# Performance work log

Hardware: AMD Instinct MI355X
Metric: run time of the kernel (lower is better)

The kernel has to match this reference:

```python
import jax, jax.numpy as jnp
import numpy as np

C = 192          # filter_channels (= in_channels in this module)
K = 3            # kernel_size
NB = 10          # num_bins of rational-quadratic spline (VITS default)
TB = 5.0         # tail_bound
NF = 4           # number of ConvFlow steps per branch
L = 3            # DDSConv n_layers
LOG2PI = float(np.log(2.0 * np.pi))


def conv1x1(x, w, b):
    # x: (B, Cin, T), w: (Cout, Cin)
    return jnp.einsum('oi,bit->bot', w, x) + b[None, :, None]


def depthwise(x, w, b, dil):
    # x: (B, C, T), w: (C, 1, K), dilated depthwise conv, 'same' padding
    pad = dil * (K - 1) // 2
    y = jax.lax.conv_general_dilated(
        x, w, window_strides=(1,), padding=[(pad, pad)], rhs_dilation=(dil,),
        dimension_numbers=('NCH', 'OIH', 'NCH'), feature_group_count=x.shape[1])
    return y + b[None, :, None]


def layer_norm_c(x, g, b, eps=1e-5):
    # VITS LayerNorm: normalize over the channel axis (axis=1)
    m = jnp.mean(x, axis=1, keepdims=True)
    v = jnp.mean((x - m) ** 2, axis=1, keepdims=True)
    return (x - m) * jax.lax.rsqrt(v + eps) * g[None, :, None] + b[None, :, None]


def dds(x, x_mask, g, dep_w, dep_b, pw_w, pw_b, ln_g, ln_b):
    # DDSConv: dilated depth-separable conv stack with residual
    if g is not None:
        x = x + g
    for i in range(L):
        dil = K ** i
        y = depthwise(x * x_mask, dep_w[i], dep_b[i], dil)
        y = jax.nn.gelu(layer_norm_c(y, ln_g[i, 0], ln_b[i, 0]))
        y = conv1x1(y, pw_w[i], pw_b[i])
        y = jax.nn.gelu(layer_norm_c(y, ln_g[i, 1], ln_b[i, 1]))
        x = x + y  # dropout disabled in deterministic reference
    return x * x_mask


def ew_affine(z, x_mask, m, logs):
    y = (m[None, :, None] + jnp.exp(logs)[None, :, None] * z) * x_mask
    ld = jnp.sum(logs[None, :, None] * x_mask, axis=(1, 2))
    return y, ld


def rqs_forward(x_in, uw, uh, ud):
    # unconstrained rational-quadratic spline, forward direction, linear tails
    mb = 1e-3  # min bin width / height / derivative
    const = float(np.log(np.expm1(1.0 - mb)))
    inside = (x_in >= -TB) & (x_in <= TB)
    ud = jnp.pad(ud, ((0, 0), (0, 0), (0, 0), (1, 1)), constant_values=const)
    wd = jax.nn.softmax(uw, -1); wd = mb + (1.0 - mb * NB) * wd
    cw = jnp.cumsum(wd, -1)
    cw = jnp.concatenate([jnp.zeros_like(cw[..., :1]), cw], -1)
    cw = 2.0 * TB * cw - TB
    cw = cw.at[..., 0].set(-TB).at[..., -1].set(TB)
    wd = cw[..., 1:] - cw[..., :-1]
    ht = jax.nn.softmax(uh, -1); ht = mb + (1.0 - mb * NB) * ht
    ch = jnp.cumsum(ht, -1)
    ch = jnp.concatenate([jnp.zeros_like(ch[..., :1]), ch], -1)
    ch = 2.0 * TB * ch - TB
    ch = ch.at[..., 0].set(-TB).at[..., -1].set(TB)
    ht = ch[..., 1:] - ch[..., :-1]
    dv = mb + jax.nn.softplus(ud)  # (..., NB+1)
    xc = jnp.clip(x_in, -TB, TB)
    idx = jnp.clip(jnp.sum((xc[..., None] >= cw[..., :-1]).astype(jnp.int32), -1) - 1, 0, NB - 1)
    g = lambda a, i: jnp.take_along_axis(a, i[..., None], -1)[..., 0]
    icw, iw, ich, ih = g(cw, idx), g(wd, idx), g(ch, idx), g(ht, idx)
    idelta = ih / iw
    d0, d1 = g(dv, idx), g(dv, idx + 1)
    th = (xc - icw) / iw
    t1m = th * (1.0 - th)
    den = idelta + (d0 + d1 - 2.0 * idelta) * t1m
    out = ich + ih * (idelta * th * th + d0 * t1m) / den
    dnum = idelta * idelta * (d1 * th * th + 2.0 * idelta * t1m + d0 * (1.0 - th) ** 2)
    lad = jnp.log(dnum) - 2.0 * jnp.log(den)
    return jnp.where(inside, out, x_in), jnp.where(inside, lad, 0.0)


def conv_flow(z, x_mask, g, pre_w, pre_b, dep_w, dep_b, pw_w, pw_b, ln_g, ln_b, proj_w, proj_b):
    x0, x1 = z[:, :1], z[:, 1:]  # (B,1,T) each
    h = conv1x1(x0, pre_w, pre_b)
    h = dds(h, x_mask, g, dep_w, dep_b, pw_w, pw_b, ln_g, ln_b)
    h = conv1x1(h, proj_w, proj_b) * x_mask      # (B, 3*NB-1, T)
    B, _, T = h.shape
    h = h.reshape(B, 1, 3 * NB - 1, T).transpose(0, 1, 3, 2)  # (B,1,T,3*NB-1)
    s = 1.0 / np.sqrt(C)
    x1n, lad = rqs_forward(x1, h[..., :NB] * s, h[..., NB:2 * NB] * s, h[..., 2 * NB:])
    zo = jnp.concatenate([x0, x1n], 1) * x_mask
    return zo, jnp.sum(lad * x_mask, axis=(1, 2))


def _forward(x, x_mask, w, e_q, pre_w, pre_b, proj_w, proj_b,
             dds_dep_w, dds_dep_b, dds_pw_w, dds_pw_b, dds_ln_g, dds_ln_b,
             post_pre_w, post_pre_b, post_proj_w, post_proj_b,
             pdds_dep_w, pdds_dep_b, pdds_pw_w, pdds_pw_b, pdds_ln_g, pdds_ln_b,
             aff_m, aff_logs,
             f_pre_w, f_pre_b, f_dep_w, f_dep_b, f_pw_w, f_pw_b, f_ln_g, f_ln_b, f_proj_w, f_proj_b,
             paff_m, paff_logs,
             p_pre_w, p_pre_b, p_dep_w, p_dep_b, p_pw_w, p_pw_b, p_ln_g, p_ln_b, p_proj_w, p_proj_b):
    x = jax.lax.stop_gradient(x)
    h = conv1x1(x, pre_w, pre_b)
    h = dds(h, x_mask, None, dds_dep_w, dds_dep_b, dds_pw_w, dds_pw_b, dds_ln_g, dds_ln_b)
    h = conv1x1(h, proj_w, proj_b) * x_mask
    hw = conv1x1(w, post_pre_w, post_pre_b)
    hw = dds(hw, x_mask, None, pdds_dep_w, pdds_dep_b, pdds_pw_w, pdds_pw_b, pdds_ln_g, pdds_ln_b)
    hw = conv1x1(hw, post_proj_w, post_proj_b) * x_mask
    e = e_q * x_mask
    zq, ldq = ew_affine(e, x_mask, paff_m, paff_logs)
    gp = h + hw
    for i in range(NF):
        zq, ld = conv_flow(zq, x_mask, gp, p_pre_w[i], p_pre_b[i], p_dep_w[i], p_dep_b[i],
                           p_pw_w[i], p_pw_b[i], p_ln_g[i], p_ln_b[i], p_proj_w[i], p_proj_b[i])
        ldq = ldq + ld
        zq = zq[:, ::-1]  # Flip (logdet 0)
    zu, z1 = zq[:, :1], zq[:, 1:]
    u = jax.nn.sigmoid(zu) * x_mask
    z0 = (w - u) * x_mask
    ldq = ldq + jnp.sum((jax.nn.log_sigmoid(zu) + jax.nn.log_sigmoid(-zu)) * x_mask, axis=(1, 2))
    logq = jnp.sum(-0.5 * (LOG2PI + e * e) * x_mask, axis=(1, 2)) - ldq
    y0 = jnp.log(jnp.maximum(z0, 1e-5)) * x_mask  # Log flow
    ldt = jnp.sum(-y0, axis=(1, 2))
    z = jnp.concatenate([y0, z1], 1)
    z, ld = ew_affine(z, x_mask, aff_m, aff_logs)
    ldt = ldt + ld
    for i in range(NF):
        z, ld = conv_flow(z, x_mask, h, f_pre_w[i], f_pre_b[i], f_dep_w[i], f_dep_b[i],
                          f_pw_w[i], f_pw_b[i], f_ln_g[i], f_ln_b[i], f_proj_w[i], f_proj_b[i])
        ldt = ldt + ld
        z = z[:, ::-1]
    nll = jnp.sum(0.5 * (LOG2PI + z * z) * x_mask, axis=(1, 2)) - ldt
    return nll + logq  # (B,)


def setup_inputs() -> dict:
    key = jax.random.key(0)
    ks = jax.random.split(key, 24)
    B, T = 32, 768
    P = 3 * NB - 1
    r = lambda k, shape, s=0.05: jax.random.normal(k, shape, jnp.float32) * s
    d = {}
    d['x'] = jax.random.normal(ks[0], (B, C, T), jnp.float32)
    d['x_mask'] = jnp.ones((B, 1, T), jnp.float32)
    d['w'] = jax.random.uniform(ks[1], (B, 1, T), jnp.float32) * 10.0 + 1.0  # positive durations
    d['e_q'] = jax.random.normal(ks[2], (B, 2, T), jnp.float32)
    d['pre_w'] = r(ks[3], (C, C)); d['pre_b'] = jnp.zeros((C,), jnp.float32)
    d['proj_w'] = r(ks[4], (C, C)); d['proj_b'] = jnp.zeros((C,), jnp.float32)
    d['dds_dep_w'] = r(ks[5], (L, C, 1, K)); d['dds_dep_b'] = jnp.zeros((L, C), jnp.float32)
    d['dds_pw_w'] = r(ks[6], (L, C, C)); d['dds_pw_b'] = jnp.zeros((L, C), jnp.float32)
    d['dds_ln_g'] = jnp.ones((L, 2, C), jnp.float32); d['dds_ln_b'] = jnp.zeros((L, 2, C), jnp.float32)
    d['post_pre_w'] = r(ks[7], (C, 1)); d['post_pre_b'] = jnp.zeros((C,), jnp.float32)
    d['post_proj_w'] = r(ks[8], (C, C)); d['post_proj_b'] = jnp.zeros((C,), jnp.float32)
    d['pdds_dep_w'] = r(ks[9], (L, C, 1, K)); d['pdds_dep_b'] = jnp.zeros((L, C), jnp.float32)
    d['pdds_pw_w'] = r(ks[10], (L, C, C)); d['pdds_pw_b'] = jnp.zeros((L, C), jnp.float32)
    d['pdds_ln_g'] = jnp.ones((L, 2, C), jnp.float32); d['pdds_ln_b'] = jnp.zeros((L, 2, C), jnp.float32)
    d['aff_m'] = r(ks[11], (2,)); d['aff_logs'] = r(ks[12], (2,))
    d['f_pre_w'] = r(ks[13], (NF, C, 1)); d['f_pre_b'] = jnp.zeros((NF, C), jnp.float32)
    d['f_dep_w'] = r(ks[14], (NF, L, C, 1, K)); d['f_dep_b'] = jnp.zeros((NF, L, C), jnp.float32)
    d['f_pw_w'] = r(ks[15], (NF, L, C, C)); d['f_pw_b'] = jnp.zeros((NF, L, C), jnp.float32)
    d['f_ln_g'] = jnp.ones((NF, L, 2, C), jnp.float32); d['f_ln_b'] = jnp.zeros((NF, L, 2, C), jnp.float32)
    d['f_proj_w'] = r(ks[16], (NF, P, C), 0.01); d['f_proj_b'] = jnp.zeros((NF, P), jnp.float32)
    d['paff_m'] = r(ks[17], (2,)); d['paff_logs'] = r(ks[18], (2,))
    d['p_pre_w'] = r(ks[19], (NF, C, 1)); d['p_pre_b'] = jnp.zeros((NF, C), jnp.float32)
    d['p_dep_w'] = r(ks[20], (NF, L, C, 1, K)); d['p_dep_b'] = jnp.zeros((NF, L, C), jnp.float32)
    d['p_pw_w'] = r(ks[21], (NF, L, C, C)); d['p_pw_b'] = jnp.zeros((NF, L, C), jnp.float32)
    d['p_ln_g'] = jnp.ones((NF, L, 2, C), jnp.float32); d['p_ln_b'] = jnp.zeros((NF, L, 2, C), jnp.float32)
    d['p_proj_w'] = r(ks[22], (NF, P, C), 0.01); d['p_proj_b'] = jnp.zeros((NF, P), jnp.float32)
    return d


def reference(x, x_mask, w, e_q, pre_w, pre_b, proj_w, proj_b,
              dds_dep_w, dds_dep_b, dds_pw_w, dds_pw_b, dds_ln_g, dds_ln_b,
              post_pre_w, post_pre_b, post_proj_w, post_proj_b,
              pdds_dep_w, pdds_dep_b, pdds_pw_w, pdds_pw_b, pdds_ln_g, pdds_ln_b,
              aff_m, aff_logs,
              f_pre_w, f_pre_b, f_dep_w, f_dep_b, f_pw_w, f_pw_b, f_ln_g, f_ln_b, f_proj_w, f_proj_b,
              paff_m, paff_logs,
              p_pre_w, p_pre_b, p_dep_w, p_dep_b, p_pw_w, p_pw_b, p_ln_g, p_ln_b, p_proj_w, p_proj_b):
    return _forward(x, x_mask, w, e_q, pre_w, pre_b, proj_w, proj_b,
                    dds_dep_w, dds_dep_b, dds_pw_w, dds_pw_b, dds_ln_g, dds_ln_b,
                    post_pre_w, post_pre_b, post_proj_w, post_proj_b,
                    pdds_dep_w, pdds_dep_b, pdds_pw_w, pdds_pw_b, pdds_ln_g, pdds_ln_b,
                    aff_m, aff_logs,
                    f_pre_w, f_pre_b, f_dep_w, f_dep_b, f_pw_w, f_pw_b, f_ln_g, f_ln_b, f_proj_w, f_proj_b,
                    paff_m, paff_logs,
                    p_pre_w, p_pre_b, p_dep_w, p_dep_b, p_pw_w, p_pw_b, p_ln_g, p_ln_b, p_proj_w, p_proj_b)
```

## Files before the change

### kernel.cpp

```cpp
#include <hip/hip_runtime.h>
#include <math.h>

#define CC 192
#define TTT 768
#define PP 29
#define LOG2PI_F 1.8378770664093453f
#define WSLOT 36864
#define PSW 6144
#define XS 200
#define XS2 196
#define PARL 1728

typedef __attribute__((ext_vector_type(8))) short short8;
typedef __attribute__((ext_vector_type(4))) float floatx4;
typedef __attribute__((ext_vector_type(2))) float float2v;
union Frag { int4 i; short8 s; };

__device__ __forceinline__ float2v fma2(float2v a, float2v b, float2v c){
  return __builtin_elementwise_fma(a, b, c);
}
__device__ __forceinline__ float geluf(float x){
  float u = 1.5957691216057308f * (x + 0.044715f*x*x*x);
  return x * __builtin_amdgcn_rcpf(1.f + __expf(-u));
}
__device__ __forceinline__ float softplus_f(float x){
  return (x > 20.f) ? x : log1pf(__expf(x));
}
__device__ __forceinline__ float logsig_f(float x){
  return -softplus_f(-x);
}
__device__ __forceinline__ unsigned short f2bf(float f){
  unsigned int u = __builtin_bit_cast(unsigned int, f);
  u += 0x7fffu + ((u >> 16) & 1u);
  return (unsigned short)(u >> 16);
}
__device__ __forceinline__ unsigned int packbf2(float a0, float a1){
  return (unsigned int)f2bf(a0) | ((unsigned int)f2bf(a1) << 16);
}
__device__ __forceinline__ void unbf2(unsigned int u, float& lo, float& hi){
  lo = __builtin_bit_cast(float, u << 16);
  hi = __builtin_bit_cast(float, u & 0xffff0000u);
}
__device__ __forceinline__ float2v unbf2v(unsigned int u){
  float2v r;
  r.x = __builtin_bit_cast(float, u << 16);
  r.y = __builtin_bit_cast(float, u & 0xffff0000u);
  return r;
}
__device__ __forceinline__ void unp8(int4 v, float* o){
  unsigned int* p = (unsigned int*)&v;
  unbf2(p[0], o[0], o[1]); unbf2(p[1], o[2], o[3]);
  unbf2(p[2], o[4], o[5]); unbf2(p[3], o[6], o[7]);
}
__device__ __forceinline__ void f4arr(float4 v, float* o){ o[0]=v.x;o[1]=v.y;o[2]=v.z;o[3]=v.w; }
__device__ __forceinline__ float2v pick2(float4 a, float4 b, int p){
  switch(p){
    case 0: return (float2v){a.x, a.y};
    case 1: return (float2v){a.z, a.w};
    case 2: return (float2v){b.x, b.y};
    default: return (float2v){b.z, b.w};
  }
}

__global__ __launch_bounds__(256) void convert_w_k(
    const float* __restrict__ p0, const float* __restrict__ p1,
    const float* __restrict__ p2, const float* __restrict__ p3,
    const float* __restrict__ p4, const float* __restrict__ p5,
    const float* __restrict__ p6, const float* __restrict__ p7,
    const float* __restrict__ p8, unsigned short* __restrict__ Wb){
  int i = blockIdx.x*256 + threadIdx.x;
  const int totalA = 33*WSLOT;
  const int total = totalA + 8*PSW;
  if (i >= total) return;
  if (i < totalA){
    int slot = i / WSLOT, j = i % WSLOT;
    int e = j & 7, lane = (j>>3) & 63, kt = j >> 9;
    int k = kt % 6, tile = kt / 6;
    int co = tile*16 + (lane & 15);
    int kk = k*32 + (lane>>4)*8 + e;
    int r = co*CC + kk;
    const float* src;
    if      (slot == 0) src = p0 + r;
    else if (slot == 1) src = p1 + r;
    else if (slot == 2) src = p2 + r;
    else if (slot < 6)  src = p3 + (size_t)(slot-3)*WSLOT + r;
    else if (slot < 9)  src = p4 + (size_t)(slot-6)*WSLOT + r;
    else if (slot < 21) src = p5 + (size_t)(slot-9)*WSLOT + r;
    else                src = p6 + (size_t)(slot-21)*WSLOT + r;
    Wb[i] = f2bf(*src);
  } else {
    int r2 = i - totalA;
    int ps = r2 / PSW, j = r2 % PSW;
    int e = j & 7, lane = (j>>3) & 63, kt = j >> 9;
    int k = kt % 6, tile = kt / 6;
    int co = tile*16 + (lane & 15); if (co > PP-1) co = PP-1;
    int kk = k*32 + (lane>>4)*8 + e;
    const float* base = (ps < 4) ? (p7 + (size_t)ps*PP*CC) : (p8 + (size_t)(ps-4)*PP*CC);
    Wb[i] = f2bf(base[co*CC + kk]);
  }
}

__global__ __launch_bounds__(256) void pack_par_k(
    const float* __restrict__ dds_dep_w, const float* __restrict__ dds_dep_b,
    const float* __restrict__ dds_ln_g,  const float* __restrict__ dds_ln_b,
    const float* __restrict__ dds_pw_b,
    const float* __restrict__ pdds_dep_w, const float* __restrict__ pdds_dep_b,
    const float* __restrict__ pdds_ln_g,  const float* __restrict__ pdds_ln_b,
    const float* __restrict__ pdds_pw_b,
    const float* __restrict__ p_dep_w, const float* __restrict__ p_dep_b,
    const float* __restrict__ p_ln_g,  const float* __restrict__ p_ln_b,
    const float* __restrict__ p_pw_b,
    const float* __restrict__ f_dep_w, const float* __restrict__ f_dep_b,
    const float* __restrict__ f_ln_g,  const float* __restrict__ f_ln_b,
    const float* __restrict__ f_pw_b,
    float* __restrict__ P){
  int i = blockIdx.x*256 + threadIdx.x;
  const int total = 30*PARL;
  if (i >= total) return;
  int ls = i / PARL, r = i % PARL;
  int arr = r / 192, c = r % 192;
  const float *dep_w, *dep_b, *ln_g, *ln_b, *pw_b;
  int l;
  if (ls < 3){
    l = ls; dep_w = dds_dep_w; dep_b = dds_dep_b; ln_g = dds_ln_g; ln_b = dds_ln_b; pw_b = dds_pw_b;
  } else if (ls < 6){
    l = ls-3; dep_w = pdds_dep_w; dep_b = pdds_dep_b; ln_g = pdds_ln_g; ln_b = pdds_ln_b; pw_b = pdds_pw_b;
  } else if (ls < 18){
    int f = (ls-6)/3; l = (ls-6)%3;
    dep_w = p_dep_w + (size_t)f*3*CC*3; dep_b = p_dep_b + (size_t)f*3*CC;
    ln_g = p_ln_g + (size_t)f*3*2*CC;  ln_b = p_ln_b + (size_t)f*3*2*CC;
    pw_b = p_pw_b + (size_t)f*3*CC;
  } else {
    int f = (ls-18)/3; l = (ls-18)%3;
    dep_w = f_dep_w + (size_t)f*3*CC*3; dep_b = f_dep_b + (size_t)f*3*CC;
    ln_g = f_ln_g + (size_t)f*3*2*CC;  ln_b = f_ln_b + (size_t)f*3*2*CC;
    pw_b = f_pw_b + (size_t)f*3*CC;
  }
  float v;
  if      (arr < 3)  v = dep_w[((size_t)l*CC + c)*3 + arr];
  else if (arr == 3) v = dep_b[(size_t)l*CC + c];
  else if (arr == 4) v = ln_g[((size_t)l*2+0)*CC + c];
  else if (arr == 5) v = ln_b[((size_t)l*2+0)*CC + c];
  else if (arr == 6) v = ln_g[((size_t)l*2+1)*CC + c];
  else if (arr == 7) v = ln_b[((size_t)l*2+1)*CC + c];
  else               v = pw_b[(size_t)l*CC + c];
  P[i] = v;
}

__global__ __launch_bounds__(256) void transpose_x_k(
    const float* __restrict__ x, unsigned short* __restrict__ xT){
  __shared__ unsigned short tile[32*XS];
  int b = blockIdx.y, t0 = blockIdx.x*32, tid = threadIdx.x;
  int tl4 = (tid & 7)*4, cr = tid >> 3;
  #pragma unroll
  for (int rnd=0; rnd<6; rnd++){
    int c = rnd*32 + cr;
    float4 v4 = *(const float4*)(x + ((size_t)b*CC + c)*TTT + t0 + tl4);
    tile[(tl4+0)*XS + c] = f2bf(v4.x);
    tile[(tl4+1)*XS + c] = f2bf(v4.y);
    tile[(tl4+2)*XS + c] = f2bf(v4.z);
    tile[(tl4+3)*XS + c] = f2bf(v4.w);
  }
  __syncthreads();
  #pragma unroll
  for (int k=0;k<3;k++){
    int task = k*256 + tid;
    int row = task/24, cn = task%24;
    *(int4*)(xT + ((size_t)b*TTT + t0 + row)*CC + cn*8) = *(const int4*)&tile[row*XS + cn*8];
  }
}

__global__ __launch_bounds__(256) void conv_cc_k(
    const unsigned short* __restrict__ in, const unsigned short* __restrict__ Wsw,
    const float* __restrict__ bias, const float* __restrict__ mask,
    const unsigned short* __restrict__ addsrc, unsigned short* __restrict__ outb, int mode){
  __shared__ unsigned short bufX[32*XS];
  __shared__ unsigned short bufY[32*XS];
  __shared__ float marr[32];
  int b = blockIdx.y, t0 = blockIdx.x*32, tid = threadIdx.x;
  #pragma unroll
  for (int k=0;k<3;k++){
    int task = k*256 + tid;
    int row = task/24, cn = task%24;
    const unsigned short* src = in + ((size_t)b*TTT + t0 + row)*CC + cn*8;
    *(int4*)&bufX[row*XS + cn*8] = *(const int4*)src;
    if (mode == 2){
      const unsigned short* s2 = addsrc + ((size_t)b*TTT + t0 + row)*CC + cn*8;
      *(int4*)&bufY[row*XS + cn*8] = *(const int4*)s2;
    }
  }
  if (tid >= 128 && tid < 160) marr[tid-128] = mask[(size_t)b*TTT + t0 + (tid-128)];
  __syncthreads();
  int w = tid >> 6, lane = tid & 63;
  int n16 = lane & 15, quad = lane >> 4;
  Frag af[3][6];
  #pragma unroll
  for (int ct=0; ct<3; ct++){
    int tile = w*3 + ct;
    #pragma unroll
    for (int k=0;k<6;k++)
      af[ct][k].i = *(const int4*)(Wsw + ((size_t)(tile*6 + k)*64 + lane)*8);
  }
  floatx4 acc[3][2];
  #pragma unroll
  for (int ct=0;ct<3;ct++)
    #pragma unroll
    for (int tt=0;tt<2;tt++)
      acc[ct][tt] = (floatx4){0.f,0.f,0.f,0.f};
  #pragma unroll
  for (int k=0;k<6;k++){
    Frag bf[2];
    #pragma unroll
    for (int tt=0;tt<2;tt++)
      bf[tt].i = *(const int4*)&bufX[(tt*16+n16)*XS + k*32 + quad*8];
    #pragma unroll
    for (int ct=0;ct<3;ct++)
      #pragma unroll
      for (int tt=0;tt<2;tt++)
        acc[ct][tt] = __builtin_amdgcn_mfma_f32_16x16x32_bf16(af[ct][k].s, bf[tt].s, acc[ct][tt], 0,0,0);
  }
  __syncthreads();
  #pragma unroll
  for (int ct=0;ct<3;ct++){
    int cobase = w*48 + ct*16 + quad*4;
    float4 b4 = *(const float4*)(bias + cobase);
    float ba[4] = {b4.x, b4.y, b4.z, b4.w};
    #pragma unroll
    for (int tt=0;tt<2;tt++){
      int t = tt*16 + n16;
      float mv = (mode >= 1) ? marr[t] : 1.f;
      float av[4] = {0.f,0.f,0.f,0.f};
      if (mode == 2){
        uint2 uy = *(uint2*)&bufY[t*XS + cobase];
        unbf2(uy.x, av[0], av[1]); unbf2(uy.y, av[2], av[3]);
      }
      float hh[4];
      #pragma unroll
      for (int r=0;r<4;r++){
        float v = acc[ct][tt][r] + ba[r];
        if (mode >= 1) v *= mv;
        if (mode == 2) v += av[r];
        hh[r] = v;
      }
      uint2 wv; wv.x = packbf2(hh[0], hh[1]); wv.y = packbf2(hh[2], hh[3]);
      *(uint2*)&bufX[t*XS + cobase] = wv;
    }
  }
  __syncthreads();
  #pragma unroll
  for (int k=0;k<3;k++){
    int task = k*256 + tid;
    int row = task/24, cn = task%24;
    *(int4*)(outb + ((size_t)b*TTT + t0 + row)*CC + cn*8) = *(const int4*)&bufX[row*XS + cn*8];
  }
}

__global__ __launch_bounds__(256,3) void mega_dds_k(
    const unsigned short* __restrict__ in,
    const float* __restrict__ zsrc, int zstride,
    const unsigned short* __restrict__ g,
    unsigned short* __restrict__ outb,
    const float* __restrict__ mask,
    const float* __restrict__ parP,
    const float* __restrict__ pw1, const float* __restrict__ pb1,
    const unsigned short* __restrict__ Wsw,
    int srcmode, int outmode,
    const unsigned short* __restrict__ projW, const float* __restrict__ projB,
    float* __restrict__ z, int zs, float* __restrict__ acco){
  __shared__ unsigned short ping[64*XS2];
  __shared__ float par[2][PARL];
  __shared__ float mrow[64];
  float* pro = par[0];

  int b = blockIdx.y, t0 = blockIdx.x*32, tid = threadIdx.x;
  int ws0 = t0 - 16;
  int w = tid >> 6, lane = tid & 63;
  int n16 = lane & 15, quad = lane >> 4;
  int row = w*16 + n16;
  const float* mkb = mask + (size_t)b*TTT;
  const int dils[3] = {1,3,9};

  if (tid < 64){
    int gt = ws0 + tid;
    bool inr = (gt >= 0) && (gt < TTT);
    int gc = gt < 0 ? 0 : (gt > TTT-1 ? TTT-1 : gt);
    mrow[tid] = inr ? mkb[gc] : 0.f;
  }
  #pragma unroll
  for (int k=0;k<7;k++){
    int i2 = k*256 + tid;
    if (i2 < PARL) par[0][i2] = parP[i2];
  }
  if (srcmode == 0){
    #pragma unroll
    for (int k=0;k<6;k++){
      int task = k*256 + tid;
      int r = task/24, cn = task%24, c0 = cn*8;
      int gt = ws0 + r;
      bool inr = (gt >= 0) && (gt < TTT);
      int gc = gt < 0 ? 0 : (gt > TTT-1 ? TTT-1 : gt);
      float mv = inr ? mkb[gc] : 0.f;
      float hv[8];
      unp8(*(const int4*)(in + ((size_t)b*TTT + gc)*CC + c0), hv);
      uint2 w0, w1;
      w0.x = packbf2(hv[0]*mv, hv[1]*mv); w0.y = packbf2(hv[2]*mv, hv[3]*mv);
      w1.x = packbf2(hv[4]*mv, hv[5]*mv); w1.y = packbf2(hv[6]*mv, hv[7]*mv);
      *(uint2*)&ping[r*XS2 + c0]     = w0;
      *(uint2*)&ping[r*XS2 + c0 + 4] = w1;
    }
  } else {
    #pragma unroll
    for (int k=0;k<6;k++){
      int task = k*256 + tid;
      int r = task/24, cn = task%24, c0 = cn*8;
      int gt = ws0 + r;
      bool inr = (gt >= 0) && (gt < TTT);
      int gc = gt < 0 ? 0 : (gt > TTT-1 ? TTT-1 : gt);
      float mv = inr ? mkb[gc] : 0.f;
      float zv = inr ? zsrc[(size_t)b*zstride + gc] : 0.f;
      float hv[8];
      if (g){
        unp8(*(const int4*)(g + ((size_t)b*TTT + gc)*CC + c0), hv);
      } else {
        #pragma unroll
        for (int e=0;e<8;e++) hv[e] = 0.f;
      }
      float4 pwa = *(const float4*)(pw1 + c0);
      float4 pwb2 = *(const float4*)(pw1 + c0 + 4);
      float4 pba = *(const float4*)(pb1 + c0);
      float4 pbb2 = *(const float4*)(pb1 + c0 + 4);
      float pwv[8], pbv[8];
      f4arr(pwa, pwv); f4arr(pwb2, pwv+4);
      f4arr(pba, pbv); f4arr(pbb2, pbv+4);
      float ov[8];
      #pragma unroll
      for (int e=0;e<8;e++) ov[e] = (hv[e] + fmaf(pwv[e], zv, pbv[e]))*mv;
      uint2 w0, w1;
      w0.x = packbf2(ov[0], ov[1]); w0.y = packbf2(ov[2], ov[3]);
      w1.x = packbf2(ov[4], ov[5]); w1.y = packbf2(ov[6], ov[7]);
      *(uint2*)&ping[r*XS2 + c0]     = w0;
      *(uint2*)&ping[r*XS2 + c0 + 4] = w1;
    }
  }
  __syncthreads();

  #pragma unroll
  for (int l=0; l<3; l++){
    const int dil = dils[l];
    const bool active = (l < 2) || (w == 1) || (w == 2);
    const float* pl = par[l & 1];
    Frag bfr[6];
    floatx4 acc[12];
    if (active){
      int iL = row - dil; iL = iL < 0 ? 0 : iL;
      int iR = row + dil; iR = iR > 63 ? 63 : iR;
      float ml = (row - dil >= 0) ? mrow[iL] : 0.f;
      float mc = mrow[row];
      float mr = (row + dil <= 63) ? mrow[iR] : 0.f;
      float2v ml2 = {ml,ml}, mc2 = {mc,mc}, mr2 = {mr,mr};
      float2v vv[24];
      float s = 0.f, q = 0.f;
      #pragma unroll
      for (int j=0;j<6;j++){
        int kk = j*32 + quad*8;
        uint2 a0 = *(uint2*)&ping[iL*XS2 + kk], a1 = *(uint2*)&ping[iL*XS2 + kk + 4];
        uint2 b0 = *(uint2*)&ping[row*XS2 + kk], b1 = *(uint2*)&ping[row*XS2 + kk + 4];
        uint2 c0v = *(uint2*)&ping[iR*XS2 + kk], c1 = *(uint2*)&ping[iR*XS2 + kk + 4];
        float2v XL[4] = {unbf2v(a0.x), unbf2v(a0.y), unbf2v(a1.x), unbf2v(a1.y)};
        float2v XC[4] = {unbf2v(b0.x), unbf2v(b0.y), unbf2v(b1.x), unbf2v(b1.y)};
        float2v XR[4] = {unbf2v(c0v.x), unbf2v(c0v.y), unbf2v(c1.x), unbf2v(c1.y)};
        float4 w0a = *(const float4*)&pl[kk],       w0b = *(const float4*)&pl[kk+4];
        float4 w1a = *(const float4*)&pl[192+kk],   w1b = *(const float4*)&pl[192+kk+4];
        float4 w2a = *(const float4*)&pl[384+kk],   w2b = *(const float4*)&pl[384+kk+4];
        float4 dba = *(const float4*)&pl[576+kk],   dbb = *(const float4*)&pl[576+kk+4];
        #pragma unroll
        for (int p=0;p<4;p++){
          float2v val = fma2(pick2(w0a,w0b,p), XL[p]*ml2,
                        fma2(pick2(w1a,w1b,p), XC[p]*mc2,
                        fma2(pick2(w2a,w2b,p), XR[p]*mr2, pick2(dba,dbb,p))));
          vv[j*4+p] = val;
          s += val.x + val.y;
          q = fmaf(val.x, val.x, fmaf(val.y, val.y, q));
        }
      }
      s += __shfl_xor(s, 16); s += __shfl_xor(s, 32);
      q += __shfl_xor(q, 16); q += __shfl_xor(q, 32);
      float mm = s*(1.f/CC);
      float rr = rsqrtf(q*(1.f/CC) - mm*mm + 1e-5f);
      {
        float2v mm2 = {mm,mm}, rr2 = {rr,rr};
        #pragma unroll
        for (int j=0;j<6;j++){
          int kk = j*32 + quad*8;
          float4 g0a = *(const float4*)&pl[768+kk], g0b = *(const float4*)&pl[768+kk+4];
          float4 b0a = *(const float4*)&pl[960+kk], b0b = *(const float4*)&pl[960+kk+4];
          unsigned int wwp[4];
          #pragma unroll
          for (int p=0;p<4;p++){
            float2v a = fma2((vv[j*4+p]-mm2)*rr2, pick2(g0a,g0b,p), pick2(b0a,b0b,p));
            wwp[p] = packbf2(geluf(a.x), geluf(a.y));
          }
          bfr[j].i = make_int4((int)wwp[0], (int)wwp[1], (int)wwp[2], (int)wwp[3]);
        }
      }
    }
    __syncthreads();
    if (l < 2){
      const float* src = parP + (size_t)(l+1)*PARL;
      #pragma unroll
      for (int k=0;k<7;k++){
        int i2 = k*256 + tid;
        if (i2 < PARL) par[(l+1)&1][i2] = src[i2];
      }
    }
    if (active){
      const unsigned short* WL = Wsw + (size_t)l*WSLOT;
      #pragma unroll
      for (int tile=0; tile<12; tile++){
        acc[tile] = (floatx4){0.f,0.f,0.f,0.f};
        Frag af[6];
        #pragma unroll
        for (int k=0;k<6;k++)
          af[k].i = *(const int4*)(WL + ((size_t)(tile*6 + k)*64 + lane)*8);
        #pragma unroll
        for (int k=0;k<6;k++)
          acc[tile] = __builtin_amdgcn_mfma_f32_16x16x32_bf16(af[k].s, bfr[k].s, acc[tile], 0,0,0);
      }
      float s2 = 0.f, q2 = 0.f;
      #pragma unroll
      for (int tile=0; tile<12; tile++){
        int co = tile*16 + quad*4;
        float4 pbv = *(const float4*)&pl[1536+co];
        float pba[4]; f4arr(pbv, pba);
        #pragma unroll
        for (int r=0;r<4;r++){
          acc[tile][r] += pba[r];
          float x = acc[tile][r];
          s2 += x; q2 = fmaf(x, x, q2);
        }
      }
      s2 += __shfl_xor(s2, 16); s2 += __shfl_xor(s2, 32);
      q2 += __shfl_xor(q2, 16); q2 += __shfl_xor(q2, 32);
      float cmP = s2*(1.f/CC);
      float crP = rsqrtf(q2*(1.f/CC) - cmP*cmP + 1e-5f);
      float2v cm2 = {cmP,cmP}, cr2 = {crP,crP};
      #pragma unroll
      for (int tile=0; tile<12; tile++){
        int co = tile*16 + quad*4;
        float4 g1v = *(const float4*)&pl[1152+co];
        float4 b1v = *(const float4*)&pl[1344+co];
        uint2 ux = *(uint2*)&ping[row*XS2 + co];
        float2v x01 = unbf2v(ux.x), x23 = unbf2v(ux.y);
        float2v v01 = {acc[tile][0], acc[tile][1]};
        float2v v23 = {acc[tile][2], acc[tile][3]};
        float2v a01 = fma2((v01-cm2)*cr2, (float2v){g1v.x,g1v.y}, (float2v){b1v.x,b1v.y});
        float2v a23 = fma2((v23-cm2)*cr2, (float2v){g1v.z,g1v.w}, (float2v){b1v.z,b1v.w});
        uint2 wv;
        wv.x = packbf2(x01.x + geluf(a01.x), x01.y + geluf(a01.y));
        wv.y = packbf2(x23.x + geluf(a23.x), x23.y + geluf(a23.y));
        *(uint2*)&ping[row*XS2 + co] = wv;
      }
    }
    __syncthreads();
  }

  if (outmode == 0){
    #pragma unroll
    for (int k=0;k<3;k++){
      int task = k*256 + tid;
      int r = task/24, cn = task%24, c0 = cn*8;
      uint2 u0 = *(uint2*)&ping[(16+r)*XS2 + c0];
      uint2 u1 = *(uint2*)&ping[(16+r)*XS2 + c0 + 4];
      *(int4*)(outb + ((size_t)b*TTT + t0 + r)*CC + c0) =
          make_int4((int)u0.x, (int)u0.y, (int)u1.x, (int)u1.y);
    }
    return;
  }

  if (w == 1 || w == 2){
    Frag bfp[6];
    #pragma unroll
    for (int k=0;k<6;k++){
      int kk = k*32 + quad*8;
      uint2 u0 = *(uint2*)&ping[row*XS2 + kk];
      uint2 u1 = *(uint2*)&ping[row*XS2 + kk + 4];
      bfp[k].i = make_int4((int)u0.x, (int)u0.y, (int)u1.x, (int)u1.y);
    }
    floatx4 acc2[2];
    acc2[0] = (floatx4){0.f,0.f,0.f,0.f};
    acc2[1] = (floatx4){0.f,0.f,0.f,0.f};
    #pragma unroll
    for (int ct2=0; ct2<2; ct2++){
      #pragma unroll
      for (int k=0;k<6;k++){
        Frag af;
        af.i = *(const int4*)(projW + ((size_t)(ct2*6 + k)*64 + lane)*8);
        acc2[ct2] = __builtin_amdgcn_mfma_f32_16x16x32_bf16(af.s, bfp[k].s, acc2[ct2], 0,0,0);
      }
    }
    int rt = row - 16;
    float mv = mrow[row];
    #pragma unroll
    for (int ct2=0; ct2<2; ct2++){
      int cobase = ct2*16 + quad*4;
      #pragma unroll
      for (int r=0;r<4;r++){
        int co = cobase + r;
        if (co < PP) pro[rt*30 + co] = (acc2[ct2][r] + projB[co]) * mv;
      }
    }
  }
  __syncthreads();
  if (tid < 32){
    const float scv = 0.07216878364870323f;
    int tg = t0 + tid;
    float m = mrow[16+tid];
    float* z0p = z + ((size_t)b*2 + zs)*TTT + tg;
    float* z1p = z + ((size_t)b*2 + (1-zs))*TTT + tg;
    float xs = *z1p;
    float uw[10], uh[10], ud[9];
    #pragma unroll
    for (int k=0;k<10;k++) uw[k]=pro[tid*30+k]*scv;
    #pragma unroll
    for (int k=0;k<10;k++) uh[k]=pro[tid*30+10+k]*scv;
    #pragma unroll
    for (int k=0;k<9;k++)  ud[k]=pro[tid*30+20+k];
    bool inside = (xs >= -5.f) && (xs <= 5.f);
    float xc = fminf(fmaxf(xs,-5.f),5.f);
    float mx=uw[0];
    #pragma unroll
    for (int k=1;k<10;k++) mx=fmaxf(mx,uw[k]);
    float sw=0.f; float wd[10];
    #pragma unroll
    for (int k=0;k<10;k++){ wd[k]=__expf(uw[k]-mx); sw+=wd[k]; }
    float invw = 1.f/sw;
    #pragma unroll
    for (int k=0;k<10;k++) wd[k]=fmaf(0.99f*invw, wd[k], 1e-3f);
    float mh=uh[0];
    #pragma unroll
    for (int k=1;k<10;k++) mh=fmaxf(mh,uh[k]);
    float sh=0.f; float ht[10];
    #pragma unroll
    for (int k=0;k<10;k++){ ht[k]=__expf(uh[k]-mh); sh+=ht[k]; }
    float invh = 1.f/sh;
    #pragma unroll
    for (int k=0;k<10;k++) ht[k]=fmaf(0.99f*invh, ht[k], 1e-3f);
    float cw=-5.f, icw=-5.f, iw=1.f; int idx=0;
    #pragma unroll
    for (int i2=0;i2<10;i2++){
      float nw = (i2==9) ? 5.f : fmaf(10.f, wd[i2], cw);
      if (cw <= xc){ idx=i2; icw=cw; iw=nw-cw; }
      cw=nw;
    }
    float ch=-5.f, ich=-5.f, ih=1.f;
    #pragma unroll
    for (int i2=0;i2<10;i2++){
      float nh = (i2==9) ? 5.f : fmaf(10.f, ht[i2], ch);
      if (i2==idx){ ich=ch; ih=nh-ch; }
      ch=nh;
    }
    const float UDC = logf(expm1f(0.999f));
    float d0=1.f, d1=1.f;
    #pragma unroll
    for (int k=0;k<11;k++){
      float uu = (k==0 || k==10) ? UDC : ud[k-1];
      float dk = 1e-3f + softplus_f(uu);
      if (k==idx)   d0=dk;
      if (k==idx+1) d1=dk;
    }
    float idel = ih/iw;
    float th = (xc-icw)/iw;
    float t1m = th*(1.f-th);
    float den = idel + (d0+d1-2.f*idel)*t1m;
    float outv = ich + ih*(idel*th*th + d0*t1m)/den;
    float omt = 1.f-th;
    float dnum = idel*idel*(d1*th*th + 2.f*idel*t1m + d0*omt*omt);
    float lad = logf(dnum) - 2.f*logf(den);
    float y = inside ? outv : xs;
    lad = inside ? lad : 0.f;
    *z1p = y*m;
    *z0p = (*z0p)*m;
    float lm = lad*m;
    lm += __shfl_xor(lm, 1); lm += __shfl_xor(lm, 2);
    lm += __shfl_xor(lm, 4); lm += __shfl_xor(lm, 8);
    lm += __shfl_xor(lm, 16);
    if (tid == 0) atomicAdd(acco + b, -lm);
  }
}

__global__ __launch_bounds__(256) void init_z_k(
    const float* __restrict__ e_q, const float* __restrict__ mask,
    const float* __restrict__ pm, const float* __restrict__ pl,
    float* __restrict__ z, float* __restrict__ acc){
  __shared__ float red[256];
  int b = blockIdx.y; int t = blockIdx.x*256 + threadIdx.x;
  float m = mask[(size_t)b*TTT + t];
  float pl0=pl[0], pl1=pl[1];
  float e0 = e_q[((size_t)b*2+0)*TTT + t]*m;
  float e1 = e_q[((size_t)b*2+1)*TTT + t]*m;
  z[((size_t)b*2+0)*TTT + t] = fmaf(__expf(pl0), e0, pm[0])*m;
  z[((size_t)b*2+1)*TTT + t] = fmaf(__expf(pl1), e1, pm[1])*m;
  float contrib = -0.5f*(LOG2PI_F + e0*e0)*m - 0.5f*(LOG2PI_F + e1*e1)*m - (pl0+pl1)*m;
  int tid = threadIdx.x;
  red[tid] = contrib;
  __syncthreads();
  for (int o=128;o>0;o>>=1){ if (tid<o) red[tid]+=red[tid+o]; __syncthreads(); }
  if (tid==0) atomicAdd(acc+b, red[0]);
}

__global__ __launch_bounds__(256) void final_pre_k(
    float* __restrict__ z, const float* __restrict__ w_in, const float* __restrict__ mask,
    const float* __restrict__ am, const float* __restrict__ al, float* __restrict__ acc){
  __shared__ float red[256];
  int b = blockIdx.y; int t = blockIdx.x*256 + threadIdx.x;
  float m = mask[(size_t)b*TTT + t];
  float zu  = z[((size_t)b*2+0)*TTT + t];
  float z1v = z[((size_t)b*2+1)*TTT + t];
  float wv  = w_in[(size_t)b*TTT + t];
  float u  = m / (1.f + __expf(-zu));
  float z0 = (wv - u)*m;
  float y0 = logf(fmaxf(z0, 1e-5f))*m;
  float al0=al[0], al1=al[1];
  z[((size_t)b*2+0)*TTT + t] = fmaf(__expf(al0), y0,  am[0])*m;
  z[((size_t)b*2+1)*TTT + t] = fmaf(__expf(al1), z1v, am[1])*m;
  float contrib = -(logsig_f(zu)+logsig_f(-zu))*m + y0 - (al0+al1)*m;
  int tid = threadIdx.x;
  red[tid] = contrib;
  __syncthreads();
  for (int o=128;o>0;o>>=1){ if (tid<o) red[tid]+=red[tid+o]; __syncthreads(); }
  if (tid==0) atomicAdd(acc+b, red[0]);
}

__global__ __launch_bounds__(256) void final_post_k(
    const float* __restrict__ z, const float* __restrict__ mask, float* __restrict__ acc){
  __shared__ float red[256];
  int b = blockIdx.y; int t = blockIdx.x*256 + threadIdx.x;
  float m = mask[(size_t)b*TTT + t];
  float z0 = z[((size_t)b*2+0)*TTT + t];
  float z1 = z[((size_t)b*2+1)*TTT + t];
  float contrib = 0.5f*(LOG2PI_F + z0*z0)*m + 0.5f*(LOG2PI_F + z1*z1)*m;
  int tid = threadIdx.x;
  red[tid] = contrib;
  __syncthreads();
  for (int o=128;o>0;o>>=1){ if (tid<o) red[tid]+=red[tid+o]; __syncthreads(); }
  if (tid==0) atomicAdd(acc+b, red[0]);
}

__global__ void write_out_k(const float* __restrict__ acc, float* __restrict__ out, int n){
  int i = threadIdx.x;
  if (i < n) out[i] = acc[i];
}

extern "C" void kernel_launch(void* const* d_in, const int* in_sizes, int n_in,
                              void* d_out, int out_size, void* d_ws, size_t ws_size,
                              hipStream_t stream){
  (void)n_in; (void)out_size; (void)ws_size;
  const float* x         = (const float*)d_in[0];
  const float* mask      = (const float*)d_in[1];
  const float* w_in      = (const float*)d_in[2];
  const float* e_q       = (const float*)d_in[3];
  const float* pre_w     = (const float*)d_in[4];
  const float* pre_b     = (const float*)d_in[5];
  const float* proj_w    = (const float*)d_in[6];
  const float* proj_b    = (const float*)d_in[7];
  const float* dds_dep_w = (const float*)d_in[8];
  const float* dds_dep_b = (const float*)d_in[9];
  const float* dds_pw_w  = (const float*)d_in[10];
  const float* dds_pw_b  = (const float*)d_in[11];
  const float* dds_ln_g  = (const float*)d_in[12];
  const float* dds_ln_b  = (const float*)d_in[13];
  const float* post_pre_w  = (const float*)d_in[14];
  const float* post_pre_b  = (const float*)d_in[15];
  const float* post_proj_w = (const float*)d_in[16];
  const float* post_proj_b = (const float*)d_in[17];
  const float* pdds_dep_w  = (const float*)d_in[18];
  const float* pdds_dep_b  = (const float*)d_in[19];
  const float* pdds_pw_w   = (const float*)d_in[20];
  const float* pdds_pw_b   = (const float*)d_in[21];
  const float* pdds_ln_g   = (const float*)d_in[22];
  const float* pdds_ln_b   = (const float*)d_in[23];
  const float* aff_m    = (const float*)d_in[24];
  const float* aff_logs = (const float*)d_in[25];
  const float* f_pre_w  = (const float*)d_in[26];
  const float* f_pre_b  = (const float*)d_in[27];
  const float* f_dep_w  = (const float*)d_in[28];
  const float* f_dep_b  = (const float*)d_in[29];
  const float* f_pw_w   = (const float*)d_in[30];
  const float* f_pw_b   = (const float*)d_in[31];
  const float* f_ln_g   = (const float*)d_in[32];
  const float* f_ln_b   = (const float*)d_in[33];
  const float* f_proj_w = (const float*)d_in[34];
  const float* f_proj_b = (const float*)d_in[35];
  const float* paff_m    = (const float*)d_in[36];
  const float* paff_logs = (const float*)d_in[37];
  const float* p_pre_w  = (const float*)d_in[38];
  const float* p_pre_b  = (const float*)d_in[39];
  const float* p_dep_w  = (const float*)d_in[40];
  const float* p_dep_b  = (const float*)d_in[41];
  const float* p_pw_w   = (const float*)d_in[42];
  const float* p_pw_b   = (const float*)d_in[43];
  const float* p_ln_g   = (const float*)d_in[44];
  const float* p_ln_b   = (const float*)d_in[45];
  const float* p_proj_w = (const float*)d_in[46];
  const float* p_proj_b = (const float*)d_in[47];

  int Bn = in_sizes[0] / (CC*TTT);
  size_t big2 = (size_t)Bn*CC*TTT;
  unsigned short* xT = (unsigned short*)d_ws;
  unsigned short* A  = xT + big2;
  unsigned short* Bb = A  + big2;
  unsigned short* H  = Bb + big2;
  unsigned short* GP = H  + big2;
  unsigned short* Wb = GP + big2;
  size_t wtot = 33*(size_t)WSLOT + 8*(size_t)PSW;
  float* parP = (float*)(Wb + ((wtot + 7) & ~(size_t)7));
  float* zbuf = parP + 30*(size_t)PARL;
  float* acc  = zbuf + (size_t)Bn*2*TTT;

  hipMemsetAsync(acc, 0, Bn*sizeof(float), stream);
  convert_w_k<<<(int)((wtot + 255)/256), 256, 0, stream>>>(
      pre_w, proj_w, post_proj_w, dds_pw_w, pdds_pw_w, p_pw_w, f_pw_w,
      p_proj_w, f_proj_w, Wb);
  pack_par_k<<<(30*PARL + 255)/256, 256, 0, stream>>>(
      dds_dep_w, dds_dep_b, dds_ln_g, dds_ln_b, dds_pw_b,
      pdds_dep_w, pdds_dep_b, pdds_ln_g, pdds_ln_b, pdds_pw_b,
      p_dep_w, p_dep_b, p_ln_g, p_ln_b, p_pw_b,
      f_dep_w, f_dep_b, f_ln_g, f_ln_b, f_pw_b, parP);

  dim3 g32(TTT/32, Bn), g256(TTT/256, Bn);
  dim3 b256(256);

  unsigned short* W_pre      = Wb + 0*(size_t)WSLOT;
  unsigned short* W_proj     = Wb + 1*(size_t)WSLOT;
  unsigned short* W_postproj = Wb + 2*(size_t)WSLOT;
  unsigned short* W_dds      = Wb + 3*(size_t)WSLOT;
  unsigned short* W_pdds     = Wb + 6*(size_t)WSLOT;
  unsigned short* W_ppw      = Wb + 9*(size_t)WSLOT;
  unsigned short* W_fpw      = Wb + 21*(size_t)WSLOT;
  unsigned short* W_pproj    = Wb + 33*(size_t)WSLOT;
  unsigned short* W_fproj    = W_pproj + 4*(size_t)PSW;

  transpose_x_k<<<g32, b256, 0, stream>>>(x, xT);

  conv_cc_k<<<g32, b256, 0, stream>>>(xT, W_pre, pre_b, mask, nullptr, A, 0);
  mega_dds_k<<<g32, b256, 0, stream>>>(A, nullptr, 0, nullptr, Bb, mask,
      parP + 0*(size_t)3*PARL, nullptr, nullptr,
      W_dds, 0, 0, nullptr, nullptr, nullptr, 0, acc);
  conv_cc_k<<<g32, b256, 0, stream>>>(Bb, W_proj, proj_b, mask, nullptr, H, 1);

  mega_dds_k<<<g32, b256, 0, stream>>>(nullptr, w_in, TTT, nullptr, A, mask,
      parP + 1*(size_t)3*PARL, post_pre_w, post_pre_b,
      W_pdds, 1, 0, nullptr, nullptr, nullptr, 0, acc);
  conv_cc_k<<<g32, b256, 0, stream>>>(A, W_postproj, post_proj_b, mask, H, GP, 2);

  init_z_k<<<g256, b256, 0, stream>>>(e_q, mask, paff_m, paff_logs, zbuf, acc);

  for (int f=0; f<4; f++){
    int s = f & 1;
    mega_dds_k<<<g32, b256, 0, stream>>>(nullptr, zbuf + (size_t)s*TTT, 2*TTT, GP, nullptr, mask,
        parP + (size_t)(2+f)*3*PARL,
        p_pre_w + (size_t)f*CC, p_pre_b + (size_t)f*CC,
        W_ppw + (size_t)f*3*WSLOT, 1, 1,
        W_pproj + (size_t)f*PSW, p_proj_b + (size_t)f*PP, zbuf, s, acc);
  }

  final_pre_k<<<g256, b256, 0, stream>>>(zbuf, w_in, mask, aff_m, aff_logs, acc);

  for (int f=0; f<4; f++){
    int s = f & 1;
    mega_dds_k<<<g32, b256, 0, stream>>>(nullptr, zbuf + (size_t)s*TTT, 2*TTT, H, nullptr, mask,
        parP + (size_t)(6+f)*3*PARL,
        f_pre_w + (size_t)f*CC, f_pre_b + (size_t)f*CC,
        W_fpw + (size_t)f*3*WSLOT, 1, 1,
        W_fproj + (size_t)f*PSW, f_proj_b + (size_t)f*PP, zbuf, s, acc);
  }

  final_post_k<<<g256, b256, 0, stream>>>(zbuf, mask, acc);
  write_out_k<<<1, 64, 0, stream>>>(acc, (float*)d_out, Bn);
}
```

Before: 776.5 us.

## Widen DDS LDS stride for 16-byte accesses, prefetch MFMA weights, fold mask into residual

The row stride of the shared ping buffer changes from 196 to 200 so every row is 16-byte aligned, and the paired 8-byte LDS reads and writes become single 128-bit accesses. The residual write now multiplies by the row mask, so the depthwise stage no longer masks its left, centre and right taps. Weight fragments for the next MFMA tile are double-buffered so global loads overlap the current tile's MFMAs. The sums for the layer-norm statistics use packed float2 math. The extra prefetch buffer raises register pressure at 3 waves per SIMD. The wider stride may also change LDS bank conflicts.

```diff
diff --git a/kernel.cpp b/kernel.cpp
--- a/kernel.cpp
+++ b/kernel.cpp
@@ -8,7 +8,7 @@
 #define WSLOT 36864
 #define PSW 6144
 #define XS 200
-#define XS2 196
+#define XSP 200
 #define PARL 1728
 
 typedef __attribute__((ext_vector_type(8))) short short8;
@@ -267,7 +267,7 @@
     int srcmode, int outmode,
     const unsigned short* __restrict__ projW, const float* __restrict__ projB,
     float* __restrict__ z, int zs, float* __restrict__ acco){
-  __shared__ unsigned short ping[64*XS2];
+  __shared__ unsigned short ping[64*XSP];
   __shared__ float par[2][PARL];
   __shared__ float mrow[64];
   float* pro = par[0];
@@ -302,11 +302,10 @@
       float mv = inr ? mkb[gc] : 0.f;
       float hv[8];
       unp8(*(const int4*)(in + ((size_t)b*TTT + gc)*CC + c0), hv);
-      uint2 w0, w1;
-      w0.x = packbf2(hv[0]*mv, hv[1]*mv); w0.y = packbf2(hv[2]*mv, hv[3]*mv);
-      w1.x = packbf2(hv[4]*mv, hv[5]*mv); w1.y = packbf2(hv[6]*mv, hv[7]*mv);
-      *(uint2*)&ping[r*XS2 + c0]     = w0;
-      *(uint2*)&ping[r*XS2 + c0 + 4] = w1;
+      int4 pk;
+      pk.x = (int)packbf2(hv[0]*mv, hv[1]*mv); pk.y = (int)packbf2(hv[2]*mv, hv[3]*mv);
+      pk.z = (int)packbf2(hv[4]*mv, hv[5]*mv); pk.w = (int)packbf2(hv[6]*mv, hv[7]*mv);
+      *(int4*)&ping[r*XSP + c0] = pk;
     }
   } else {
     #pragma unroll
@@ -335,11 +334,10 @@
       float ov[8];
       #pragma unroll
       for (int e=0;e<8;e++) ov[e] = (hv[e] + fmaf(pwv[e], zv, pbv[e]))*mv;
-      uint2 w0, w1;
-      w0.x = packbf2(ov[0], ov[1]); w0.y = packbf2(ov[2], ov[3]);
-      w1.x = packbf2(ov[4], ov[5]); w1.y = packbf2(ov[6], ov[7]);
-      *(uint2*)&ping[r*XS2 + c0]     = w0;
-      *(uint2*)&ping[r*XS2 + c0 + 4] = w1;
+      int4 pk;
+      pk.x = (int)packbf2(ov[0], ov[1]); pk.y = (int)packbf2(ov[2], ov[3]);
+      pk.z = (int)packbf2(ov[4], ov[5]); pk.w = (int)packbf2(ov[6], ov[7]);
+      *(int4*)&ping[r*XSP + c0] = pk;
     }
   }
   __syncthreads();
@@ -354,35 +352,32 @@
     if (active){
       int iL = row - dil; iL = iL < 0 ? 0 : iL;
       int iR = row + dil; iR = iR > 63 ? 63 : iR;
-      float ml = (row - dil >= 0) ? mrow[iL] : 0.f;
-      float mc = mrow[row];
-      float mr = (row + dil <= 63) ? mrow[iR] : 0.f;
-      float2v ml2 = {ml,ml}, mc2 = {mc,mc}, mr2 = {mr,mr};
       float2v vv[24];
-      float s = 0.f, q = 0.f;
+      float2v s2v = {0.f,0.f}, q2v = {0.f,0.f};
       #pragma unroll
       for (int j=0;j<6;j++){
         int kk = j*32 + quad*8;
-        uint2 a0 = *(uint2*)&ping[iL*XS2 + kk], a1 = *(uint2*)&ping[iL*XS2 + kk + 4];
-        uint2 b0 = *(uint2*)&ping[row*XS2 + kk], b1 = *(uint2*)&ping[row*XS2 + kk + 4];
-        uint2 c0v = *(uint2*)&ping[iR*XS2 + kk], c1 = *(uint2*)&ping[iR*XS2 + kk + 4];
-        float2v XL[4] = {unbf2v(a0.x), unbf2v(a0.y), unbf2v(a1.x), unbf2v(a1.y)};
-        float2v XC[4] = {unbf2v(b0.x), unbf2v(b0.y), unbf2v(b1.x), unbf2v(b1.y)};
-        float2v XR[4] = {unbf2v(c0v.x), unbf2v(c0v.y), unbf2v(c1.x), unbf2v(c1.y)};
+        int4 L4 = *(const int4*)&ping[iL*XSP + kk];
+        int4 C4 = *(const int4*)&ping[row*XSP + kk];
+        int4 R4 = *(const int4*)&ping[iR*XSP + kk];
+        unsigned int* Lp = (unsigned int*)&L4;
+        unsigned int* Cp = (unsigned int*)&C4;
+        unsigned int* Rp = (unsigned int*)&R4;
         float4 w0a = *(const float4*)&pl[kk],       w0b = *(const float4*)&pl[kk+4];
         float4 w1a = *(const float4*)&pl[192+kk],   w1b = *(const float4*)&pl[192+kk+4];
         float4 w2a = *(const float4*)&pl[384+kk],   w2b = *(const float4*)&pl[384+kk+4];
         float4 dba = *(const float4*)&pl[576+kk],   dbb = *(const float4*)&pl[576+kk+4];
         #pragma unroll
         for (int p=0;p<4;p++){
-          float2v val = fma2(pick2(w0a,w0b,p), XL[p]*ml2,
-                        fma2(pick2(w1a,w1b,p), XC[p]*mc2,
-                        fma2(pick2(w2a,w2b,p), XR[p]*mr2, pick2(dba,dbb,p))));
+          float2v val = fma2(pick2(w0a,w0b,p), unbf2v(Lp[p]),
+                        fma2(pick2(w1a,w1b,p), unbf2v(Cp[p]),
+                        fma2(pick2(w2a,w2b,p), unbf2v(Rp[p]), pick2(dba,dbb,p))));
           vv[j*4+p] = val;
-          s += val.x + val.y;
-          q = fmaf(val.x, val.x, fmaf(val.y, val.y, q));
+          s2v += val;
+          q2v = fma2(val, val, q2v);
         }
       }
+      float s = s2v.x + s2v.y, q = q2v.x + q2v.y;
       s += __shfl_xor(s, 16); s += __shfl_xor(s, 32);
       q += __shfl_xor(q, 16); q += __shfl_xor(q, 32);
       float mm = s*(1.f/CC);
@@ -415,50 +410,61 @@
     }
     if (active){
       const unsigned short* WL = Wsw + (size_t)l*WSLOT;
+      Frag afb[2][6];
+      #pragma unroll
+      for (int k=0;k<6;k++)
+        afb[0][k].i = *(const int4*)(WL + ((size_t)(0*6 + k)*64 + lane)*8);
       #pragma unroll
       for (int tile=0; tile<12; tile++){
+        int cur = tile & 1, nxt = cur ^ 1;
+        if (tile < 11){
+          #pragma unroll
+          for (int k=0;k<6;k++)
+            afb[nxt][k].i = *(const int4*)(WL + ((size_t)((tile+1)*6 + k)*64 + lane)*8);
+        }
         acc[tile] = (floatx4){0.f,0.f,0.f,0.f};
-        Frag af[6];
         #pragma unroll
         for (int k=0;k<6;k++)
-          af[k].i = *(const int4*)(WL + ((size_t)(tile*6 + k)*64 + lane)*8);
-        #pragma unroll
-        for (int k=0;k<6;k++)
-          acc[tile] = __builtin_amdgcn_mfma_f32_16x16x32_bf16(af[k].s, bfr[k].s, acc[tile], 0,0,0);
-      }
-      float s2 = 0.f, q2 = 0.f;
+          acc[tile] = __builtin_amdgcn_mfma_f32_16x16x32_bf16(afb[cur][k].s, bfr[k].s, acc[tile], 0,0,0);
+      }
+      float2v s2p = {0.f,0.f}, q2p = {0.f,0.f};
       #pragma unroll
       for (int tile=0; tile<12; tile++){
         int co = tile*16 + quad*4;
         float4 pbv = *(const float4*)&pl[1536+co];
-        float pba[4]; f4arr(pbv, pba);
-        #pragma unroll
-        for (int r=0;r<4;r++){
-          acc[tile][r] += pba[r];
-          float x = acc[tile][r];
-          s2 += x; q2 = fmaf(x, x, q2);
-        }
-      }
+        acc[tile][0] += pbv.x; acc[tile][1] += pbv.y;
+        acc[tile][2] += pbv.z; acc[tile][3] += pbv.w;
+        float2v v01 = {acc[tile][0], acc[tile][1]};
+        float2v v23 = {acc[tile][2], acc[tile][3]};
+        s2p += v01 + v23;
+        q2p = fma2(v01, v01, q2p);
+        q2p = fma2(v23, v23, q2p);
+      }
+      float s2 = s2p.x + s2p.y, q2 = q2p.x + q2p.y;
       s2 += __shfl_xor(s2, 16); s2 += __shfl_xor(s2, 32);
       q2 += __shfl_xor(q2, 16); q2 += __shfl_xor(q2, 32);
       float cmP = s2*(1.f/CC);
       float crP = rsqrtf(q2*(1.f/CC) - cmP*cmP + 1e-5f);
+      float mc = mrow[row];
+      float2v mc2 = {mc,mc};
       float2v cm2 = {cmP,cmP}, cr2 = {crP,crP};
       #pragma unroll
       for (int tile=0; tile<12; tile++){
         int co = tile*16 + quad*4;
         float4 g1v = *(const float4*)&pl[1152+co];
         float4 b1v = *(const float4*)&pl[1344+co];
-        uint2 ux = *(uint2*)&ping[row*XS2 + co];
+        uint2 ux = *(uint2*)&ping[row*XSP + co];
         float2v x01 = unbf2v(ux.x), x23 = unbf2v(ux.y);
         float2v v01 = {acc[tile][0], acc[tile][1]};
         float2v v23 = {acc[tile][2], acc[tile][3]};
         float2v a01 = fma2((v01-cm2)*cr2, (float2v){g1v.x,g1v.y}, (float2v){b1v.x,b1v.y});
         float2v a23 = fma2((v23-cm2)*cr2, (float2v){g1v.z,g1v.w}, (float2v){b1v.z,b1v.w});
+        float2v h01 = (x01 + (float2v){geluf(a01.x), geluf(a01.y)}) * mc2;
+        float2v h23 = (x23 + (float2v){geluf(a23.x), geluf(a23.y)}) * mc2;
         uint2 wv;
-        wv.x = packbf2(x01.x + geluf(a01.x), x01.y + geluf(a01.y));
-        wv.y = packbf2(x23.x + geluf(a23.x), x23.y + geluf(a23.y));
-        *(uint2*)&ping[row*XS2 + co] = wv;
+        wv.x = packbf2(h01.x, h01.y);
+        wv.y = packbf2(h23.x, h23.y);
+        *(uint2*)&ping[row*XSP + co] = wv;
       }
     }
     __syncthreads();
@@ -469,10 +475,7 @@
     for (int k=0;k<3;k++){
       int task = k*256 + tid;
       int r = task/24, cn = task%24, c0 = cn*8;
-      uint2 u0 = *(uint2*)&ping[(16+r)*XS2 + c0];
-      uint2 u1 = *(uint2*)&ping[(16+r)*XS2 + c0 + 4];
-      *(int4*)(outb + ((size_t)b*TTT + t0 + r)*CC + c0) =
-          make_int4((int)u0.x, (int)u0.y, (int)u1.x, (int)u1.y);
+      *(int4*)(outb + ((size_t)b*TTT + t0 + r)*CC + c0) = *(const int4*)&ping[(16+r)*XSP + c0];
     }
     return;
   }
@@ -480,12 +483,8 @@
   if (w == 1 || w == 2){
     Frag bfp[6];
     #pragma unroll
-    for (int k=0;k<6;k++){
-      int kk = k*32 + quad*8;
-      uint2 u0 = *(uint2*)&ping[row*XS2 + kk];
-      uint2 u1 = *(uint2*)&ping[row*XS2 + kk + 4];
-      bfp[k].i = make_int4((int)u0.x, (int)u0.y, (int)u1.x, (int)u1.y);
-    }
+    for (int k=0;k<6;k++)
+      bfp[k].i = *(const int4*)&ping[row*XSP + k*32 + quad*8];
     floatx4 acc2[2];
     acc2[0] = (floatx4){0.f,0.f,0.f,0.f};
     acc2[1] = (floatx4){0.f,0.f,0.f,0.f};
```

Result: faster. 745.0 us (-4.1%).
